# Kernel tuning notes

Measured on AMD Instinct MI355X. Metric: run time of the kernel, lower is better.

Reference implementation:

```python
import jax, jax.numpy as jnp
import numpy as np

B, C, HEADS, D, DKQ = 1024, 512, 8, 64, 8
DV = C // HEADS                 # 64, dim_head_v
QKVC = DV + 2 * DKQ             # 80, qkv channels per head
EPS = 1e-5


def _bn(x, g, b, m, v):
    # eval-mode batchnorm, channel axis = 1
    shp = (1, -1) + (1,) * (x.ndim - 2)
    scale = g.reshape(shp) / jnp.sqrt(v.reshape(shp) + EPS)
    return (x - m.reshape(shp)) * scale + b.reshape(shp)


def _rel_index():
    i = np.arange(D)
    # key_index - query_index + D - 1, row-major flatten -> (D*D,)
    return jnp.asarray((i[:, None] - i[None, :] + D - 1).reshape(-1))


def setup_inputs() -> dict:
    key = jax.random.key(0)
    ks = jax.random.split(key, 16)
    O = HEADS * QKVC
    d = {
        "x": jax.random.normal(ks[0], (B, C, D), jnp.float32),
        "conv_w": jax.random.normal(ks[1], (O, C), jnp.float32) * 0.02,
        "bn1_g": jax.random.normal(ks[2], (O,), jnp.float32) * 0.1 + 1.0,
        "bn1_b": jax.random.normal(ks[3], (O,), jnp.float32) * 0.1,
        "bn1_m": jax.random.normal(ks[4], (O,), jnp.float32) * 0.1,
        "bn1_v": jax.random.uniform(ks[5], (O,), jnp.float32) * 0.5 + 0.5,
        "rel": jax.random.normal(ks[6], (QKVC, 2 * D - 1), jnp.float32),
        "bn2_g": jax.random.normal(ks[7], (3 * HEADS,), jnp.float32) * 0.1 + 1.0,
        "bn2_b": jax.random.normal(ks[8], (3 * HEADS,), jnp.float32) * 0.1,
        "bn2_m": jax.random.normal(ks[9], (3 * HEADS,), jnp.float32) * 0.1,
        "bn2_v": jax.random.uniform(ks[10], (3 * HEADS,), jnp.float32) * 0.5 + 0.5,
        "bn3_g": jax.random.normal(ks[11], (2 * C,), jnp.float32) * 0.1 + 1.0,
        "bn3_b": jax.random.normal(ks[12], (2 * C,), jnp.float32) * 0.1,
        "bn3_m": jax.random.normal(ks[13], (2 * C,), jnp.float32) * 0.1,
        "bn3_v": jax.random.uniform(ks[14], (2 * C,), jnp.float32) * 0.5 + 0.5,
    }
    return d


def reference(x, conv_w, bn1_g, bn1_b, bn1_m, bn1_v, rel,
              bn2_g, bn2_b, bn2_m, bn2_v, bn3_g, bn3_b, bn3_m, bn3_v):
    # 1x1 conv1d + BN1d: [B, O, D]
    qkv = jnp.einsum('oc,bcd->bod', conv_w, x)
    qkv = _bn(qkv, bn1_g, bn1_b, bn1_m, bn1_v)
    # rearrange 'b (q h) d -> b h q d' with q=QKVC, h=HEADS (channel = q*H + h)
    qkv = qkv.reshape(B, QKVC, HEADS, D).transpose(0, 2, 1, 3)  # [B,H,QKVC,D]
    q = qkv[:, :, :DKQ]                # [B,H,DKQ,D]
    k = qkv[:, :, DKQ:2 * DKQ]         # [B,H,DKQ,D]
    v = qkv[:, :, 2 * DKQ:]            # [B,H,DV,D]

    # relative positional embeddings gathered from table
    emb = rel[:, _rel_index()].reshape(QKVC, D, D)
    r_q, r_k, r_v = emb[:DKQ], emb[DKQ:2 * DKQ], emb[2 * DKQ:]

    qr = jnp.einsum('bhid,idj->bhdj', q, r_q)
    kr = jnp.einsum('bhid,idj->bhdj', k, r_k)
    dots = jnp.einsum('bhid,bhij->bhdj', q, k)

    # rearrange 'n b h d j -> b (h n) d j'  (channel = h*3 + n)
    stacked = jnp.stack([qr, kr, dots], axis=2).reshape(B, 3 * HEADS, D, D)
    stacked = _bn(stacked, bn2_g, bn2_b, bn2_m, bn2_v)
    norm_dots = stacked.reshape(B, HEADS, 3, D, D).sum(axis=2)  # [B,H,D,D]

    attn = jax.nn.softmax(norm_dots, axis=-1)
    out = jnp.einsum('bhdj,bhij->bhid', attn, v)      # [B,H,DV,D]
    kv = jnp.einsum('bhdj,idj->bhid', attn, r_v)      # [B,H,DV,D]

    # rearrange 'n b h i d -> b (n h i) d'  (channel = n*H*DV + h*DV + i)
    st = jnp.stack([kv, out], axis=1).reshape(B, 2 * HEADS * DV, D)
    st = _bn(st, bn3_g, bn3_b, bn3_m, bn3_v)
    return st.reshape(B, 2, HEADS * DV, D).sum(axis=1)  # [B,C,D]
```

## Files before the change

### kernel.cpp

```cpp
#include <hip/hip_runtime.h>
#include <hip/hip_bf16.h>

#define B_    1024
#define C_    512
#define H_    8
#define D_    64
#define EPS_  1e-5f

typedef __attribute__((ext_vector_type(4))) float f32x4;
typedef __attribute__((ext_vector_type(8))) short bf16x8;
typedef __attribute__((ext_vector_type(8))) unsigned short u16x8;

__device__ __forceinline__ float bf2f(unsigned short h) {
    union { unsigned int u; float f; } c;
    c.u = ((unsigned int)h) << 16;
    return c.f;
}
__device__ __forceinline__ unsigned short f2bf(float f) {
    __hip_bfloat16 h = __float2bfloat16(f);
    return *reinterpret_cast<unsigned short*>(&h);
}

#define KBAR() do { \
    asm volatile("s_waitcnt lgkmcnt(0)" ::: "memory"); \
    __builtin_amdgcn_s_barrier(); \
} while (0)

__global__ __launch_bounds__(256) void k0_prep(
    const float* __restrict__ w, const float* __restrict__ rel,
    const float* __restrict__ g2, const float* __restrict__ v2,
    const float* __restrict__ g3, const float* __restrict__ v3,
    unsigned short* __restrict__ wf, unsigned short* __restrict__ relB,
    unsigned short* __restrict__ relvA)
{
    if (blockIdx.x < 160) {
        int t = blockIdx.x * 256 + threadIdx.x;
        int o  = t >> 6;
        int c0 = (t & 63) * 8;
        const float* src = w + (size_t)o * C_ + c0;
        u16x8 p;
#pragma unroll
        for (int e = 0; e < 8; ++e) p[e] = f2bf(src[e]);
        int f = (o >> 4) * 16 + (c0 >> 5);
        int l = (o & 15) | (((c0 >> 3) & 3) << 4);
        *reinterpret_cast<u16x8*>(&wf[(size_t)f * 512 + l * 8]) = p;
        return;
    }
    int tid = (blockIdx.x - 160) * 256 + threadIdx.x;
    if (tid < 4096) {
        int h = tid >> 9, uf = (tid >> 6) & 7, l = tid & 63;
        int u = uf * 16 + (l & 15);
        int g = l >> 4;
        float sq = g2[3*h]     * rsqrtf(v2[3*h]     + EPS_);
        float sk = g2[3*h + 1] * rsqrtf(v2[3*h + 1] + EPS_);
        u16x8 p;
#pragma unroll
        for (int e = 0; e < 8; ++e) {
            int s = g * 8 + e;
            float val = 0.f;
            if (u < 127 && s < 16)
                val = (s < 8 ? sq : sk) * rel[s * 127 + u];
            p[e] = f2bf(val);
        }
        *reinterpret_cast<u16x8*>(&relB[(size_t)tid * 8]) = p;
    } else if (tid < 4096 + 8192) {
        int t2 = tid - 4096;
        int h = t2 >> 10, iF = (t2 >> 8) & 3, tt = (t2 >> 6) & 3, l = t2 & 63;
        int i = iF * 16 + (l & 15);
        int c3 = h * 64 + i;
        float scl = g3[c3] * rsqrtf(v3[c3] + EPS_);
        const float* rrow = rel + (size_t)(16 + i) * 127;
        u16x8 p;
#pragma unroll
        for (int e = 0; e < 8; ++e) {
            int u = (l >> 4) * 8 + e + 32 * tt;
            p[e] = f2bf((u < 127) ? scl * rrow[u] : 0.f);
        }
        *reinterpret_cast<u16x8*>(&relvA[(size_t)t2 * 8]) = p;
    }
}

#define LDW1 72

struct K1Ctx {
    const float* xb;
    const unsigned short* wf;
    unsigned short (*xt)[64 * LDW1];
    int wv, lane, lm, lg, cp, c4;
};

template<int KT>
__device__ __forceinline__ void k1_step(const K1Ctx& c, f32x4 (&acc)[5][4],
                                        bf16x8 (&afu)[10], bf16x8 (&afp)[10])
{
    if (KT < 7) {
#pragma unroll
        for (int i = 0; i < 10; ++i) {
            int fm = i % 5, ks = i / 5;
            size_t f = (size_t)((c.wv * 5 + fm) * 16 + (KT + 1) * 2 + ks) * 512;
            afp[i] = *reinterpret_cast<const bf16x8*>(&c.wf[f + c.lane * 8]);
        }
    }
    f32x4 pa, pc;
    if (KT < 7) {
        pa = *reinterpret_cast<const f32x4*>(&c.xb[((KT + 1) * 64 + 2 * c.cp) * 64 + c.c4]);
        pc = *reinterpret_cast<const f32x4*>(&c.xb[((KT + 1) * 64 + 2 * c.cp + 1) * 64 + c.c4]);
    }
#pragma unroll
    for (int ks = 0; ks < 2; ++ks) {
        bf16x8 bfr[4];
#pragma unroll
        for (int fn = 0; fn < 4; ++fn)
            bfr[fn] = *reinterpret_cast<const bf16x8*>(
                &c.xt[KT & 1][(fn * 16 + c.lm) * LDW1 + ks * 32 + c.lg * 8]);
#pragma unroll
        for (int fm = 0; fm < 5; ++fm)
#pragma unroll
            for (int fn = 0; fn < 4; ++fn)
                acc[fm][fn] = __builtin_amdgcn_mfma_f32_16x16x32_bf16(
                    afu[ks * 5 + fm], bfr[fn], acc[fm][fn], 0, 0, 0);
    }
    if (KT < 7) {
#pragma unroll
        for (int j = 0; j < 4; ++j) {
            unsigned int pk = (unsigned int)f2bf(pa[j]) | ((unsigned int)f2bf(pc[j]) << 16);
            *reinterpret_cast<unsigned int*>(
                &c.xt[(KT & 1) ^ 1][(c.c4 + j) * LDW1 + 2 * c.cp]) = pk;
        }
    }
    KBAR();
}

__global__ __launch_bounds__(512) void k1_gemm(
    const float* __restrict__ x, const unsigned short* __restrict__ wf,
    const float* __restrict__ g1, const float* __restrict__ b1,
    const float* __restrict__ m1, const float* __restrict__ v1,
    const float* __restrict__ g3, const float* __restrict__ v3,
    unsigned short* __restrict__ qkA, unsigned short* __restrict__ vB)
{
    __shared__ unsigned short xt[2][64 * LDW1];
    __shared__ float ssc[640], ssh[640];

    const int tid = threadIdx.x;
    const int b   = blockIdx.x;

    for (int t = tid; t < 640; t += 512) {
        float sc = g1[t] * rsqrtf(v1[t] + EPS_);
        float sh = b1[t] - m1[t] * sc;
        int cc = t >> 3, hh = t & 7;
        if (cc >= 16) {
            int c3 = 512 + hh * 64 + (cc - 16);
            float f = g3[c3] * rsqrtf(v3[c3] + EPS_);
            sc *= f; sh *= f;
        }
        ssc[t] = sc;
        ssh[t] = sh;
    }

    K1Ctx c;
    c.xb   = x + (size_t)b * C_ * D_;
    c.wf   = wf;
    c.xt   = xt;
    c.lane = tid & 63;
    c.wv   = tid >> 6;
    c.lm   = c.lane & 15;
    c.lg   = c.lane >> 4;
    c.cp   = tid >> 4;
    c.c4   = (tid & 15) * 4;

    f32x4 acc[5][4];
#pragma unroll
    for (int i = 0; i < 5; ++i)
#pragma unroll
        for (int j = 0; j < 4; ++j) acc[i][j] = (f32x4){0.f, 0.f, 0.f, 0.f};

    bf16x8 afA[10], afB[10];
#pragma unroll
    for (int i = 0; i < 10; ++i) {
        int fm = i % 5, ks = i / 5;
        size_t f = (size_t)((c.wv * 5 + fm) * 16 + ks) * 512;
        afA[i] = *reinterpret_cast<const bf16x8*>(&wf[f + c.lane * 8]);
    }
    {
        f32x4 a = *reinterpret_cast<const f32x4*>(&c.xb[(2 * c.cp) * 64 + c.c4]);
        f32x4 d = *reinterpret_cast<const f32x4*>(&c.xb[(2 * c.cp + 1) * 64 + c.c4]);
#pragma unroll
        for (int j = 0; j < 4; ++j) {
            unsigned int pk = (unsigned int)f2bf(a[j]) | ((unsigned int)f2bf(d[j]) << 16);
            *reinterpret_cast<unsigned int*>(&xt[0][(c.c4 + j) * LDW1 + 2 * c.cp]) = pk;
        }
    }
    KBAR();

    k1_step<0>(c, acc, afA, afB);
    k1_step<1>(c, acc, afB, afA);
    k1_step<2>(c, acc, afA, afB);
    k1_step<3>(c, acc, afB, afA);
    k1_step<4>(c, acc, afA, afB);
    k1_step<5>(c, acc, afB, afA);
    k1_step<6>(c, acc, afA, afB);
    k1_step<7>(c, acc, afB, afA);

    const int wv = c.wv, lm = c.lm, lg = c.lg;
#pragma unroll
    for (int fm = 0; fm < 5; ++fm) {
#pragma unroll
        for (int fn = 0; fn < 4; ++fn) {
            int d = fn * 16 + lm;
#pragma unroll
            for (int r = 0; r < 4; ++r) {
                int o = wv * 80 + fm * 16 + lg * 4 + r;
                int cc = o >> 3, hh = o & 7;
                float val = acc[fm][fn][r] * ssc[o] + ssh[o];
                unsigned short bv = f2bf(val);
                if (cc < 8)
                    qkA[(((size_t)b * 8 + hh) * 4 + (d >> 4)) * 256 + (d & 15) * 8 + cc] = bv;
                else if (cc < 16)
                    qkA[(((size_t)b * 8 + hh) * 4 + (d >> 4)) * 256 + ((d & 15) + 16) * 8 + (cc - 8)] = bv;
                else
                    vB[((size_t)(b * 8 + hh) * 64 + (cc - 16)) * 64 + d] = bv;
            }
        }
    }
}

#define SGP 84
#define SA  72
#define RLD 136

__global__ __launch_bounds__(256) void k2_attn(
    const unsigned short* __restrict__ qkA, const unsigned short* __restrict__ vB,
    const unsigned short* __restrict__ relB, const unsigned short* __restrict__ relvA,
    const float* __restrict__ g2, const float* __restrict__ v2,
    const float* __restrict__ g3, const float* __restrict__ b3,
    const float* __restrict__ m3, const float* __restrict__ v3,
    float* __restrict__ outp)
{
    __shared__ float          SGb[64 * SGP];
    __shared__ unsigned short attn[64 * SA];
    __shared__ unsigned short A2[64 * RLD];
    __shared__ float sh3[64];

    const int tid  = threadIdx.x;
    const int b    = blockIdx.x >> 3;
    const int h    = blockIdx.x & 7;
    const int lane = tid & 63;
    const int w    = tid >> 6;
    const int lmm  = lane & 15;
    const int lg   = lane >> 4;

    const unsigned short* qbase = qkA + ((size_t)(b * 8 + h) * 4) * 256;

    for (int i = tid; i < 64 * RLD / 2; i += 256)
        reinterpret_cast<unsigned int*>(A2)[i] = 0u;
    if (tid < 64) {
        int c = h * 64 + tid;
        float sa = g3[c] * rsqrtf(v3[c] + EPS_);
        float sb = g3[512 + c] * rsqrtf(v3[512 + c] + EPS_);
        sh3[tid] = (b3[c] - m3[c] * sa) + (b3[512 + c] - m3[512 + c] * sb);
    }
    const float s_dt = g2[3 * h + 2] * rsqrtf(v2[3 * h + 2] + EPS_);

    const int uf_lo = (w == 0) ? 0 : ((16 * w - 15) >> 4);
    const int uf_hi_raw = (16 * w + 78) >> 4;
    const int uf_hi = uf_hi_raw > 7 ? 7 : uf_hi_raw;

    bf16x8 zv = {0, 0, 0, 0, 0, 0, 0, 0};
    bf16x8 aA = zv;
    if (lane < 32)
        aA = *reinterpret_cast<const bf16x8*>(&qbase[w * 256 + lane * 8]);
    bf16x8 kBf[4];
#pragma unroll
    for (int jf = 0; jf < 4; ++jf) {
        kBf[jf] = zv;
        if (lane < 16)
            kBf[jf] = *reinterpret_cast<const bf16x8*>(&qbase[jf * 256 + (lane + 16) * 8]);
    }
    bf16x8 rBf[8];
#pragma unroll
    for (int uf = 0; uf < 8; ++uf) {
        rBf[uf] = zv;
        if (uf >= uf_lo && uf <= uf_hi)
            rBf[uf] = *reinterpret_cast<const bf16x8*>(
                &relB[(size_t)(h * 8 + uf) * 512 + lane * 8]);
    }

    f32x4 dotsAcc[4];
#pragma unroll
    for (int jf = 0; jf < 4; ++jf)
        dotsAcc[jf] = __builtin_amdgcn_mfma_f32_16x16x32_bf16(
            aA, kBf[jf], (f32x4){0.f, 0.f, 0.f, 0.f}, 0, 0, 0);
    f32x4 sgAcc[8];
#pragma unroll
    for (int uf = 0; uf < 8; ++uf) {
        sgAcc[uf] = (f32x4){0.f, 0.f, 0.f, 0.f};
        if (uf >= uf_lo && uf <= uf_hi)
            sgAcc[uf] = __builtin_amdgcn_mfma_f32_16x16x32_bf16(
                aA, rBf[uf], sgAcc[uf], 0, 0, 0);
    }

#pragma unroll
    for (int uf = 0; uf < 8; ++uf) {
        if (uf < uf_lo || uf > uf_hi) continue;
#pragma unroll
        for (int r = 0; r < 4; ++r) {
            int d = (w << 4) + (lg << 2) + r;
            int t = uf * 16 + lmm - d + 15;
            if (t >= 0 && t < 79)
                SGb[d * SGP + t] = sgAcc[uf][r];
        }
    }
    __syncthreads();

#pragma unroll
    for (int r = 0; r < 4; ++r) {
        int d = (w << 4) + (lg << 2) + r;
        const float* sgr = &SGb[d * SGP];
        float sc0 = s_dt * dotsAcc[0][r] + sgr[78 - lmm];
        float sc1 = s_dt * dotsAcc[1][r] + sgr[62 - lmm];
        float sc2 = s_dt * dotsAcc[2][r] + sgr[46 - lmm];
        float sc3 = s_dt * dotsAcc[3][r] + sgr[30 - lmm];
        float mx = fmaxf(fmaxf(sc0, sc1), fmaxf(sc2, sc3));
        mx = fmaxf(mx, __shfl_xor(mx, 1));
        mx = fmaxf(mx, __shfl_xor(mx, 2));
        mx = fmaxf(mx, __shfl_xor(mx, 4));
        mx = fmaxf(mx, __shfl_xor(mx, 8));
        float e0 = __expf(sc0 - mx), e1 = __expf(sc1 - mx);
        float e2 = __expf(sc2 - mx), e3 = __expf(sc3 - mx);
        float sum = (e0 + e1) + (e2 + e3);
        sum += __shfl_xor(sum, 1);
        sum += __shfl_xor(sum, 2);
        sum += __shfl_xor(sum, 4);
        sum += __shfl_xor(sum, 8);
        float inv = 1.f / sum;
        unsigned short p0 = f2bf(e0 * inv), p1 = f2bf(e1 * inv);
        unsigned short p2 = f2bf(e2 * inv), p3 = f2bf(e3 * inv);
        attn[d * SA + lmm]      = p0;
        attn[d * SA + 16 + lmm] = p1;
        attn[d * SA + 32 + lmm] = p2;
        attn[d * SA + 48 + lmm] = p3;
        A2[d * RLD + 63 + d - lmm] = p0;
        A2[d * RLD + 47 + d - lmm] = p1;
        A2[d * RLD + 31 + d - lmm] = p2;
        A2[d * RLD + 15 + d - lmm] = p3;
    }

    const int lk8  = lg * 8;
    const int irow = (w << 4) + lmm;
    const unsigned short* vbase = vB + (size_t)(b * 8 + h) * 4096;
    bf16x8 av0 = *reinterpret_cast<const bf16x8*>(&vbase[irow * 64 + lk8]);
    bf16x8 av1 = *reinterpret_cast<const bf16x8*>(&vbase[irow * 64 + 32 + lk8]);
    bf16x8 rvA[4];
#pragma unroll
    for (int t = 0; t < 4; ++t)
        rvA[t] = *reinterpret_cast<const bf16x8*>(
            &relvA[(size_t)(((h * 4 + w) * 4 + t)) * 512 + lane * 8]);

    __syncthreads();

    f32x4 acc[4];
#pragma unroll
    for (int nf = 0; nf < 4; ++nf) acc[nf] = (f32x4){0.f, 0.f, 0.f, 0.f};

#pragma unroll
    for (int nf = 0; nf < 4; ++nf) {
        const unsigned short* arow = &attn[(nf * 16 + lmm) * SA + lk8];
        acc[nf] = __builtin_amdgcn_mfma_f32_16x16x32_bf16(
            av0, *reinterpret_cast<const bf16x8*>(&arow[0]), acc[nf], 0, 0, 0);
        acc[nf] = __builtin_amdgcn_mfma_f32_16x16x32_bf16(
            av1, *reinterpret_cast<const bf16x8*>(&arow[32]), acc[nf], 0, 0, 0);
        const unsigned short* a2row = &A2[(nf * 16 + lmm) * RLD + lk8];
        acc[nf] = __builtin_amdgcn_mfma_f32_16x16x32_bf16(
            rvA[0], *reinterpret_cast<const bf16x8*>(&a2row[0]), acc[nf], 0, 0, 0);
        acc[nf] = __builtin_amdgcn_mfma_f32_16x16x32_bf16(
            rvA[1], *reinterpret_cast<const bf16x8*>(&a2row[32]), acc[nf], 0, 0, 0);
        acc[nf] = __builtin_amdgcn_mfma_f32_16x16x32_bf16(
            rvA[2], *reinterpret_cast<const bf16x8*>(&a2row[64]), acc[nf], 0, 0, 0);
        acc[nf] = __builtin_amdgcn_mfma_f32_16x16x32_bf16(
            rvA[3], *reinterpret_cast<const bf16x8*>(&a2row[96]), acc[nf], 0, 0, 0);
    }

    float* op = outp + ((size_t)b * 512 + h * 64) * 64;
    const int r0 = lg * 4;
#pragma unroll
    for (int r = 0; r < 4; ++r) {
        int i = (w << 4) + r0 + r;
        float sh = sh3[i];
#pragma unroll
        for (int nf = 0; nf < 4; ++nf)
            op[(size_t)i * 64 + nf * 16 + lmm] = acc[nf][r] + sh;
    }
}

extern "C" void kernel_launch(void* const* d_in, const int* in_sizes, int n_in,
                              void* d_out, int out_size, void* d_ws, size_t ws_size,
                              hipStream_t stream) {
    (void)in_sizes; (void)n_in; (void)out_size; (void)ws_size;
    const float* x   = (const float*)d_in[0];
    const float* w   = (const float*)d_in[1];
    const float* g1  = (const float*)d_in[2];
    const float* b1  = (const float*)d_in[3];
    const float* m1  = (const float*)d_in[4];
    const float* v1  = (const float*)d_in[5];
    const float* rel = (const float*)d_in[6];
    const float* g2  = (const float*)d_in[7];
    const float* b2  = (const float*)d_in[8];  (void)b2;
    const float* m2  = (const float*)d_in[9];  (void)m2;
    const float* v2  = (const float*)d_in[10];
    const float* g3  = (const float*)d_in[11];
    const float* b3  = (const float*)d_in[12];
    const float* m3  = (const float*)d_in[13];
    const float* v3  = (const float*)d_in[14];
    float* out = (float*)d_out;

    unsigned short* wfrag = (unsigned short*)d_ws;
    unsigned short* relB  = (unsigned short*)((char*)d_ws + 655360);
    unsigned short* relvA = (unsigned short*)((char*)d_ws + 720896);
    unsigned short* qkA   = (unsigned short*)((char*)d_ws + 1048576);
    unsigned short* vB    = (unsigned short*)((char*)d_ws + 1048576 + (size_t)16777216);

    hipLaunchKernelGGL(k0_prep, dim3(208), dim3(256), 0, stream,
                       w, rel, g2, v2, g3, v3, wfrag, relB, relvA);
    hipLaunchKernelGGL(k1_gemm, dim3(1024), dim3(512), 0, stream,
                       x, wfrag, g1, b1, m1, v1, g3, v3, qkA, vB);
    hipLaunchKernelGGL(k2_attn, dim3(8192), dim3(256), 0, stream,
                       qkA, vB, relB, relvA, g2, v2, g3, b3, m3, v3, out);
}
```

Baseline: 164.0 us.

## Split k1 GEMM output rows across two 256-thread blocks per batch

The projection GEMM now launches two blocks per batch element, each with 4 waves covering half of the 640 output rows, in place of one 512-thread block covering all rows. Each thread stages twice as many x elements into shared memory, and the weight fragment pointer and BN scale tables are offset per half. The aim is more, smaller blocks for better occupancy and scheduling across CUs. The cost is that each batch's x tile is read and converted to bf16 twice.

Measured after the change: 182.8 us. 11.4% more time.

```diff
diff --git a/kernel.cpp b/kernel.cpp
--- a/kernel.cpp
+++ b/kernel.cpp
@@ -101,10 +101,12 @@
             afp[i] = *reinterpret_cast<const bf16x8*>(&c.wf[f + c.lane * 8]);
         }
     }
-    f32x4 pa, pc;
+    f32x4 pa, pc, pa2, pc2;
     if (KT < 7) {
-        pa = *reinterpret_cast<const f32x4*>(&c.xb[((KT + 1) * 64 + 2 * c.cp) * 64 + c.c4]);
-        pc = *reinterpret_cast<const f32x4*>(&c.xb[((KT + 1) * 64 + 2 * c.cp + 1) * 64 + c.c4]);
+        pa  = *reinterpret_cast<const f32x4*>(&c.xb[((KT + 1) * 64 + 2 * c.cp) * 64 + c.c4]);
+        pc  = *reinterpret_cast<const f32x4*>(&c.xb[((KT + 1) * 64 + 2 * c.cp + 1) * 64 + c.c4]);
+        pa2 = *reinterpret_cast<const f32x4*>(&c.xb[((KT + 1) * 64 + 2 * (c.cp + 16)) * 64 + c.c4]);
+        pc2 = *reinterpret_cast<const f32x4*>(&c.xb[((KT + 1) * 64 + 2 * (c.cp + 16) + 1) * 64 + c.c4]);
     }
 #pragma unroll
     for (int ks = 0; ks < 2; ++ks) {
@@ -126,12 +128,15 @@
             unsigned int pk = (unsigned int)f2bf(pa[j]) | ((unsigned int)f2bf(pc[j]) << 16);
             *reinterpret_cast<unsigned int*>(
                 &c.xt[(KT & 1) ^ 1][(c.c4 + j) * LDW1 + 2 * c.cp]) = pk;
+            unsigned int pk2 = (unsigned int)f2bf(pa2[j]) | ((unsigned int)f2bf(pc2[j]) << 16);
+            *reinterpret_cast<unsigned int*>(
+                &c.xt[(KT & 1) ^ 1][(c.c4 + j) * LDW1 + 2 * (c.cp + 16)]) = pk2;
         }
     }
     KBAR();
 }
 
-__global__ __launch_bounds__(512) void k1_gemm(
+__global__ __launch_bounds__(256) void k1_gemm(
     const float* __restrict__ x, const unsigned short* __restrict__ wf,
     const float* __restrict__ g1, const float* __restrict__ b1,
     const float* __restrict__ m1, const float* __restrict__ v1,
@@ -139,15 +144,18 @@
     unsigned short* __restrict__ qkA, unsigned short* __restrict__ vB)
 {
     __shared__ unsigned short xt[2][64 * LDW1];
-    __shared__ float ssc[640], ssh[640];
-
-    const int tid = threadIdx.x;
-    const int b   = blockIdx.x;
-
-    for (int t = tid; t < 640; t += 512) {
-        float sc = g1[t] * rsqrtf(v1[t] + EPS_);
-        float sh = b1[t] - m1[t] * sc;
-        int cc = t >> 3, hh = t & 7;
+    __shared__ float ssc[320], ssh[320];
+
+    const int tid  = threadIdx.x;
+    const int b    = blockIdx.x >> 1;
+    const int mh   = blockIdx.x & 1;
+    const int row0 = mh * 320;
+
+    for (int t = tid; t < 320; t += 256) {
+        int o = row0 + t;
+        float sc = g1[o] * rsqrtf(v1[o] + EPS_);
+        float sh = b1[o] - m1[o] * sc;
+        int cc = o >> 3, hh = o & 7;
         if (cc >= 16) {
             int c3 = 512 + hh * 64 + (cc - 16);
             float f = g3[c3] * rsqrtf(v3[c3] + EPS_);
@@ -159,7 +167,7 @@
 
     K1Ctx c;
     c.xb   = x + (size_t)b * C_ * D_;
-    c.wf   = wf;
+    c.wf   = wf + (size_t)(mh * 20) * 16 * 512;
     c.xt   = xt;
     c.lane = tid & 63;
     c.wv   = tid >> 6;
@@ -179,15 +187,19 @@
     for (int i = 0; i < 10; ++i) {
         int fm = i % 5, ks = i / 5;
         size_t f = (size_t)((c.wv * 5 + fm) * 16 + ks) * 512;
-        afA[i] = *reinterpret_cast<const bf16x8*>(&wf[f + c.lane * 8]);
+        afA[i] = *reinterpret_cast<const bf16x8*>(&c.wf[f + c.lane * 8]);
     }
     {
-        f32x4 a = *reinterpret_cast<const f32x4*>(&c.xb[(2 * c.cp) * 64 + c.c4]);
-        f32x4 d = *reinterpret_cast<const f32x4*>(&c.xb[(2 * c.cp + 1) * 64 + c.c4]);
+        f32x4 a  = *reinterpret_cast<const f32x4*>(&c.xb[(2 * c.cp) * 64 + c.c4]);
+        f32x4 d  = *reinterpret_cast<const f32x4*>(&c.xb[(2 * c.cp + 1) * 64 + c.c4]);
+        f32x4 a2 = *reinterpret_cast<const f32x4*>(&c.xb[(2 * (c.cp + 16)) * 64 + c.c4]);
+        f32x4 d2 = *reinterpret_cast<const f32x4*>(&c.xb[(2 * (c.cp + 16) + 1) * 64 + c.c4]);
 #pragma unroll
         for (int j = 0; j < 4; ++j) {
             unsigned int pk = (unsigned int)f2bf(a[j]) | ((unsigned int)f2bf(d[j]) << 16);
             *reinterpret_cast<unsigned int*>(&xt[0][(c.c4 + j) * LDW1 + 2 * c.cp]) = pk;
+            unsigned int pk2 = (unsigned int)f2bf(a2[j]) | ((unsigned int)f2bf(d2[j]) << 16);
+            *reinterpret_cast<unsigned int*>(&xt[0][(c.c4 + j) * LDW1 + 2 * (c.cp + 16)]) = pk2;
         }
     }
     KBAR();
@@ -209,9 +221,10 @@
             int d = fn * 16 + lm;
 #pragma unroll
             for (int r = 0; r < 4; ++r) {
-                int o = wv * 80 + fm * 16 + lg * 4 + r;
+                int rl = wv * 80 + fm * 16 + lg * 4 + r;
+                int o  = row0 + rl;
                 int cc = o >> 3, hh = o & 7;
-                float val = acc[fm][fn][r] * ssc[o] + ssh[o];
+                float val = acc[fm][fn][r] * ssc[rl] + ssh[rl];
                 unsigned short bv = f2bf(val);
                 if (cc < 8)
                     qkA[(((size_t)b * 8 + hh) * 4 + (d >> 4)) * 256 + (d & 15) * 8 + cc] = bv;
@@ -421,7 +434,7 @@
 
     hipLaunchKernelGGL(k0_prep, dim3(208), dim3(256), 0, stream,
                        w, rel, g2, v2, g3, v3, wfrag, relB, relvA);
-    hipLaunchKernelGGL(k1_gemm, dim3(1024), dim3(512), 0, stream,
+    hipLaunchKernelGGL(k1_gemm, dim3(2048), dim3(256), 0, stream,
                        x, wfrag, g1, b1, m1, v1, g3, v3, qkA, vB);
     hipLaunchKernelGGL(k2_attn, dim3(8192), dim3(256), 0, stream,
                        qkA, vB, relB, relvA, g2, v2, g3, b3, m3, v3, out);
```
